# Performance work log

Hardware: AMD Instinct MI355X
Metric: run time of the kernel (lower is better)

The kernel has to match this reference:

```python
import jax, jax.numpy as jnp
import numpy as np

ALPHA = 1.0

def setup_inputs() -> dict:
    key = jax.random.key(0)
    k1, k2, k3, k4 = jax.random.split(key, 4)
    B, N, D = 2048, 32768, 128
    return {
        "anchor": jax.random.normal(k1, (B, D), dtype=jnp.float32),
        "positive": jax.random.normal(k2, (B, D), dtype=jnp.float32),
        "negative": jax.random.normal(k3, (N, D), dtype=jnp.float32),
        "r_score": jax.random.normal(k4, (B, 1), dtype=jnp.float32),
    }

def reference(anchor, positive, negative, r_score):
    # pos_sim: [B,1] elementwise dot per row
    pos_sim = jnp.sum(anchor * positive, axis=1, keepdims=True)
    # neg_mul: [B,N] score matrix; row-wise stable logsumexp -> [B,1]
    neg_mul = jnp.matmul(anchor, negative.T)
    neg_sim = jax.scipy.special.logsumexp(neg_mul, axis=1, keepdims=True)
    loss = jax.nn.relu(neg_sim - pos_sim + r_score + ALPHA)
    return jnp.mean(loss)
```

## Files before the change

kernel.cpp:

```cpp
#include <hip/hip_runtime.h>
#include <hip/hip_bf16.h>


#define B_ROWS 2048
#define N_NEG  32768
#define DIM    128
#define LOG2E  1.4426950408889634f
#define LN2    0.6931471805599453f

typedef __bf16 bf16x8 __attribute__((ext_vector_type(8)));
typedef float  f32x4  __attribute__((ext_vector_type(4)));

static __device__ inline unsigned short f2bf(float f) {
    union { float f; unsigned u; } v; v.f = f;
    unsigned r = v.u + 0x7FFF + ((v.u >> 16) & 1);
    return (unsigned short)(r >> 16);
}

static __device__ inline void pin(bf16x8& v) {
    f32x4 t = __builtin_bit_cast(f32x4, v);
    asm volatile("" : "+v"(t));
    v = __builtin_bit_cast(bf16x8, t);
}

__global__ void prep(const float* __restrict__ anchor,
                     const float* __restrict__ positive,
                     const float* __restrict__ neg,
                     unsigned short* __restrict__ a_bf,
                     unsigned short* __restrict__ n_bf,
                     float* __restrict__ pos_sim,
                     float* __restrict__ out) {
    int t = threadIdx.x;
    if (blockIdx.x < 256) {
        if (blockIdx.x == 0 && t == 0) out[0] = 0.0f;
        int row = blockIdx.x * 8 + (t >> 5);
        int c4  = (t & 31) * 4;
        const float4 a4 = *(const float4*)(anchor   + row * DIM + c4);
        const float4 p4 = *(const float4*)(positive + row * DIM + c4);
        float dot = a4.x * p4.x + a4.y * p4.y + a4.z * p4.z + a4.w * p4.w;
        ushort4 ab;
        ab.x = f2bf(a4.x * LOG2E); ab.y = f2bf(a4.y * LOG2E);
        ab.z = f2bf(a4.z * LOG2E); ab.w = f2bf(a4.w * LOG2E);
        *(ushort4*)(a_bf + row * DIM + c4) = ab;
        #pragma unroll
        for (int m = 1; m <= 16; m <<= 1) dot += __shfl_xor(dot, m, 64);
        if ((t & 31) == 0) pos_sim[row] = dot;
    } else {
        int i = (blockIdx.x - 256) * 256 + t;
        #pragma unroll
        for (int k = 0; k < 4; k++) {
            int idx = i + k * (1024 * 256);
            float4 v = *(const float4*)(neg + (size_t)idx * 4);
            ushort4 o;
            o.x = f2bf(v.x); o.y = f2bf(v.y); o.z = f2bf(v.z); o.w = f2bf(v.w);
            *(ushort4*)(n_bf + (size_t)idx * 4) = o;
        }
    }
}

__global__ __launch_bounds__(256, 2) void fused_gemm_lse(
        const unsigned short* __restrict__ A,
        const unsigned short* __restrict__ Nb,
        float* __restrict__ partial) {
    __shared__ float sLDS[4][64];

    const int tid  = threadIdx.x;
    const int wave = tid >> 6, lane = tid & 63;
    const int q = lane >> 4, c = lane & 15;
    const int cc = blockIdx.x & 15;
    const int rg = blockIdx.x >> 4;

    bf16x8 af[4][4];
    const unsigned short* Ab = A + (size_t)rg * 64 * DIM;
    #pragma unroll
    for (int i = 0; i < 4; i++)
        #pragma unroll
        for (int k = 0; k < 4; k++)
            af[i][k] = *(const bf16x8*)(Ab + (i * 16 + c) * DIM + k * 32 + q * 8);
    #pragma unroll
    for (int i = 0; i < 4; i++)
        #pragma unroll
        for (int k = 0; k < 4; k++)
            pin(af[i][k]);

    const unsigned short* Bb = Nb + ((size_t)cc * 2048 + wave * 512 + c) * DIM + q * 8;
    const f32x4 zero4 = {0.f, 0.f, 0.f, 0.f};
    f32x4 sumacc[4] = {zero4, zero4, zero4, zero4};

    #pragma unroll 2
    for (int ct = 0; ct < 32; ct++) {
        const unsigned short* Bt = Bb + ct * 16 * DIM;
        bf16x8 bf[4];
        #pragma unroll
        for (int k = 0; k < 4; k++)
            bf[k] = *(const bf16x8*)(Bt + k * 32);
        #pragma unroll
        for (int i = 0; i < 4; i++) {
            f32x4 acc = __builtin_amdgcn_mfma_f32_16x16x32_bf16(af[i][0], bf[0], zero4, 0, 0, 0);
            acc = __builtin_amdgcn_mfma_f32_16x16x32_bf16(af[i][1], bf[1], acc, 0, 0, 0);
            acc = __builtin_amdgcn_mfma_f32_16x16x32_bf16(af[i][2], bf[2], acc, 0, 0, 0);
            acc = __builtin_amdgcn_mfma_f32_16x16x32_bf16(af[i][3], bf[3], acc, 0, 0, 0);
            sumacc[i][0] += __builtin_amdgcn_exp2f(acc[0]);
            sumacc[i][1] += __builtin_amdgcn_exp2f(acc[1]);
            sumacc[i][2] += __builtin_amdgcn_exp2f(acc[2]);
            sumacc[i][3] += __builtin_amdgcn_exp2f(acc[3]);
        }
    }

    #pragma unroll
    for (int i = 0; i < 4; i++) {
        #pragma unroll
        for (int r = 0; r < 4; r++) {
            float v = sumacc[i][r];
            v += __shfl_xor(v, 1, 64);
            v += __shfl_xor(v, 2, 64);
            v += __shfl_xor(v, 4, 64);
            v += __shfl_xor(v, 8, 64);
            sumacc[i][r] = v;
        }
        if (c == 0)
            *(f32x4*)&sLDS[wave][i * 16 + q * 4] = sumacc[i];
    }
    __syncthreads();
    if (tid < 64) {
        float s = sLDS[0][tid] + sLDS[1][tid] + sLDS[2][tid] + sLDS[3][tid];
        partial[cc * 2048 + rg * 64 + tid] = s;
    }
}

__global__ void finalize(const float* __restrict__ partial,
                         const float* __restrict__ pos_sim,
                         const float* __restrict__ r_score,
                         float* __restrict__ out) {
    __shared__ float red[4];
    const int tid  = threadIdx.x;
    const int wave = tid >> 6, lane = tid & 63;
    const int row  = blockIdx.x * 256 + tid;

    float se = 0.0f;
    #pragma unroll
    for (int ccp = 0; ccp < 16; ccp++)
        se += partial[ccp * 2048 + row];
    float loss = __log2f(se) * LN2 - pos_sim[row] + r_score[row] + 1.0f;
    float acc  = fmaxf(loss, 0.0f);
    #pragma unroll
    for (int m = 1; m <= 32; m <<= 1) acc += __shfl_xor(acc, m, 64);
    if (lane == 0) red[wave] = acc;
    __syncthreads();
    if (tid == 0)
        atomicAdd(out, (red[0] + red[1] + red[2] + red[3]) * (1.0f / (float)B_ROWS));
}

extern "C" void kernel_launch(void* const* d_in, const int* in_sizes, int n_in,
                              void* d_out, int out_size, void* d_ws, size_t ws_size,
                              hipStream_t stream) {
    const float* anchor   = (const float*)d_in[0];
    const float* positive = (const float*)d_in[1];
    const float* negative = (const float*)d_in[2];
    const float* r_score  = (const float*)d_in[3];
    float* out = (float*)d_out;

    char* ws = (char*)d_ws;
    float* pos_sim       = (float*)ws;
    float* partial       = (float*)(ws + 8192);
    unsigned short* a_bf = (unsigned short*)(ws + 8192 + 131072);
    unsigned short* n_bf = (unsigned short*)(ws + 8192 + 131072 + 524288);

    prep<<<1280, 256, 0, stream>>>(anchor, positive, negative, a_bf, n_bf,
                                   pos_sim, out);
    fused_gemm_lse<<<512, 256, 0, stream>>>(a_bf, n_bf, partial);
    finalize<<<8, 256, 0, stream>>>(partial, pos_sim, r_score, out);
}
```

Before: 110.0 us.

## Stage negative tiles through swizzled LDS with async double buffering and 128-row A tiles

Each block now holds 128 anchor rows in registers instead of 64, which doubles reuse of every negative tile loaded. Negative tiles are streamed into per-wave LDS double buffers with global_load_lds, using an XOR swizzle to avoid bank conflicts, and the next tile is prefetched while the current one is computed. The column split becomes 32 chunks of 1024, so there are twice as many partial sums to reduce. The trade-off is higher VGPR pressure from the 8x4 A fragments, which may cut occupancy under launch_bounds(256,2), plus hand-written vmcnt waits that must match the number of outstanding loads.

Measured after the change: 99.57 us. 1.1x faster.

```diff
diff --git a/kernel.cpp b/kernel.cpp
--- a/kernel.cpp
+++ b/kernel.cpp
@@ -21,6 +21,13 @@
     f32x4 t = __builtin_bit_cast(f32x4, v);
     asm volatile("" : "+v"(t));
     v = __builtin_bit_cast(bf16x8, t);
+}
+
+static __device__ inline void load_lds16(const void* g, void* s) {
+    __builtin_amdgcn_global_load_lds(
+        (const __attribute__((address_space(1))) void*)g,
+        (__attribute__((address_space(3))) void*)s,
+        16, 0, 0);
 }
 
 __global__ void prep(const float* __restrict__ anchor,
@@ -62,53 +69,82 @@
         const unsigned short* __restrict__ A,
         const unsigned short* __restrict__ Nb,
         float* __restrict__ partial) {
-    __shared__ float sLDS[4][64];
+    __shared__ unsigned short bbuf[4][2][4096];
+    __shared__ float sLDS[4][128];
 
     const int tid  = threadIdx.x;
     const int wave = tid >> 6, lane = tid & 63;
     const int q = lane >> 4, c = lane & 15;
-    const int cc = blockIdx.x & 15;
-    const int rg = blockIdx.x >> 4;
-
-    bf16x8 af[4][4];
-    const unsigned short* Ab = A + (size_t)rg * 64 * DIM;
-    #pragma unroll
-    for (int i = 0; i < 4; i++)
+    const int cc = blockIdx.x & 31;
+    const int rg = blockIdx.x >> 5;
+
+    bf16x8 af[8][4];
+    const unsigned short* Ab = A + (size_t)rg * 128 * DIM;
+    #pragma unroll
+    for (int i = 0; i < 8; i++)
         #pragma unroll
         for (int k = 0; k < 4; k++)
             af[i][k] = *(const bf16x8*)(Ab + (i * 16 + c) * DIM + k * 32 + q * 8);
     #pragma unroll
-    for (int i = 0; i < 4; i++)
+    for (int i = 0; i < 8; i++)
         #pragma unroll
         for (int k = 0; k < 4; k++)
             pin(af[i][k]);
 
-    const unsigned short* Bb = Nb + ((size_t)cc * 2048 + wave * 512 + c) * DIM + q * 8;
+    const int off_e = q * DIM + ((c ^ q) << 3);
+    const int off_o = q * DIM + ((c ^ (q + 4)) << 3);
+
+    int rck[4];
+    #pragma unroll
+    for (int k = 0; k < 4; k++) rck[k] = (((k * 4 + q) ^ (c & 7)) << 4);
+
+    const unsigned short* Bw = Nb + ((size_t)cc * 1024 + wave * 256) * DIM;
+    unsigned short* sb0 = &bbuf[wave][0][0];
+    unsigned short* sb1 = &bbuf[wave][1][0];
+
+    #pragma unroll
+    for (int i = 0; i < 8; i++)
+        load_lds16(Bw + i * 512 + ((i & 1) ? off_o : off_e), sb0 + i * 512);
+
     const f32x4 zero4 = {0.f, 0.f, 0.f, 0.f};
-    f32x4 sumacc[4] = {zero4, zero4, zero4, zero4};
-
-    #pragma unroll 2
-    for (int ct = 0; ct < 32; ct++) {
-        const unsigned short* Bt = Bb + ct * 16 * DIM;
-        bf16x8 bf[4];
-        #pragma unroll
-        for (int k = 0; k < 4; k++)
-            bf[k] = *(const bf16x8*)(Bt + k * 32);
-        #pragma unroll
-        for (int i = 0; i < 4; i++) {
-            f32x4 acc = __builtin_amdgcn_mfma_f32_16x16x32_bf16(af[i][0], bf[0], zero4, 0, 0, 0);
-            acc = __builtin_amdgcn_mfma_f32_16x16x32_bf16(af[i][1], bf[1], acc, 0, 0, 0);
-            acc = __builtin_amdgcn_mfma_f32_16x16x32_bf16(af[i][2], bf[2], acc, 0, 0, 0);
-            acc = __builtin_amdgcn_mfma_f32_16x16x32_bf16(af[i][3], bf[3], acc, 0, 0, 0);
-            sumacc[i][0] += __builtin_amdgcn_exp2f(acc[0]);
-            sumacc[i][1] += __builtin_amdgcn_exp2f(acc[1]);
-            sumacc[i][2] += __builtin_amdgcn_exp2f(acc[2]);
-            sumacc[i][3] += __builtin_amdgcn_exp2f(acc[3]);
-        }
-    }
-
-    #pragma unroll
-    for (int i = 0; i < 4; i++) {
+    f32x4 sumacc[8];
+    #pragma unroll
+    for (int i = 0; i < 8; i++) sumacc[i] = zero4;
+
+    for (int t = 0; t < 8; t++) {
+        const unsigned short* cur = (t & 1) ? sb1 : sb0;
+        if (t < 7) {
+            const unsigned short* Bt = Bw + (size_t)(t + 1) * 32 * DIM;
+            unsigned short* nx = (t & 1) ? sb0 : sb1;
+            #pragma unroll
+            for (int i = 0; i < 8; i++)
+                load_lds16(Bt + i * 512 + ((i & 1) ? off_o : off_e), nx + i * 512);
+            asm volatile("s_waitcnt vmcnt(8)" ::: "memory");
+        } else {
+            asm volatile("s_waitcnt vmcnt(0)" ::: "memory");
+        }
+        #pragma unroll
+        for (int j = 0; j < 2; j++) {
+            bf16x8 bf[4];
+            #pragma unroll
+            for (int k = 0; k < 4; k++)
+                bf[k] = *(const bf16x8*)((const char*)cur + (j * 16 + c) * 256 + rck[k]);
+            #pragma unroll
+            for (int i = 0; i < 8; i++) {
+                f32x4 acc = __builtin_amdgcn_mfma_f32_16x16x32_bf16(af[i][0], bf[0], zero4, 0, 0, 0);
+                acc = __builtin_amdgcn_mfma_f32_16x16x32_bf16(af[i][1], bf[1], acc, 0, 0, 0);
+                acc = __builtin_amdgcn_mfma_f32_16x16x32_bf16(af[i][2], bf[2], acc, 0, 0, 0);
+                acc = __builtin_amdgcn_mfma_f32_16x16x32_bf16(af[i][3], bf[3], acc, 0, 0, 0);
+                sumacc[i][0] += __builtin_amdgcn_exp2f(acc[0]);
+                sumacc[i][1] += __builtin_amdgcn_exp2f(acc[1]);
+                sumacc[i][2] += __builtin_amdgcn_exp2f(acc[2]);
+                sumacc[i][3] += __builtin_amdgcn_exp2f(acc[3]);
+            }
+        }
+    }
+
+    #pragma unroll
+    for (int i = 0; i < 8; i++) {
         #pragma unroll
         for (int r = 0; r < 4; r++) {
             float v = sumacc[i][r];
@@ -122,9 +158,9 @@
             *(f32x4*)&sLDS[wave][i * 16 + q * 4] = sumacc[i];
     }
     __syncthreads();
-    if (tid < 64) {
+    if (tid < 128) {
         float s = sLDS[0][tid] + sLDS[1][tid] + sLDS[2][tid] + sLDS[3][tid];
-        partial[cc * 2048 + rg * 64 + tid] = s;
+        partial[cc * 2048 + rg * 128 + tid] = s;
     }
 }
 
@@ -139,7 +175,7 @@
 
     float se = 0.0f;
     #pragma unroll
-    for (int ccp = 0; ccp < 16; ccp++)
+    for (int ccp = 0; ccp < 32; ccp++)
         se += partial[ccp * 2048 + row];
     float loss = __log2f(se) * LN2 - pos_sim[row] + r_score[row] + 1.0f;
     float acc  = fmaxf(loss, 0.0f);
@@ -163,8 +199,8 @@
     char* ws = (char*)d_ws;
     float* pos_sim       = (float*)ws;
     float* partial       = (float*)(ws + 8192);
-    unsigned short* a_bf = (unsigned short*)(ws + 8192 + 131072);
-    unsigned short* n_bf = (unsigned short*)(ws + 8192 + 131072 + 524288);
+    unsigned short* a_bf = (unsigned short*)(ws + 8192 + 262144);
+    unsigned short* n_bf = (unsigned short*)(ws + 8192 + 262144 + 524288);
 
     prep<<<1280, 256, 0, stream>>>(anchor, positive, negative, a_bf, n_bf,
                                    pos_sim, out);
```
